# Performance work log

Hardware: AMD Instinct MI355X
Metric: run time of the kernel (lower is better)

The kernel has to match this reference:

```python
import jax, jax.numpy as jnp
import numpy as np

# Multi-level grid resolutions (module constants from init_kwargs)
RESO_3D = [16, 32, 64]
RESO_2D = [64, 128, 256]
EPS = 1e-9


def _corners(D):
    # binary corner offsets, shape (2**D, D)
    c = np.stack(np.meshgrid(*([np.arange(2)] * D), indexing='ij'), axis=-1).reshape(-1, D)
    return jnp.asarray(c, dtype=jnp.int32)


def _coords_weights(xyz, reso):
    # xyz in [0,1), shape (N, D). Returns flat voxel idx (N, 2**D) and trilinear weights (N, 2**D).
    D = xyz.shape[1]
    corners = _corners(D)                                   # (C, D)
    x = xyz * (reso - 1)
    x0 = jnp.floor(x)
    frac = x - x0                                           # (N, D)
    x0 = x0.astype(jnp.int32)
    cc = jnp.clip(x0[:, None, :] + corners[None], 0, reso - 1)   # (N, C, D)
    w = jnp.prod(jnp.where(corners[None] == 1, frac[:, None, :], 1.0 - frac[:, None, :]), axis=-1)  # (N, C)
    strides = (reso ** jnp.arange(D - 1, -1, -1)).astype(jnp.int32)  # row-major
    idx = jnp.sum(cc * strides, axis=-1)                    # (N, C)
    return idx, w


def _grid_create(xyz, feat, reso):
    # Scatter-splat: weighted-average point features into a dense level grid (reso**D, F).
    N, D = xyz.shape
    F = feat.shape[1]
    idx, w = _coords_weights(xyz, reso)                     # (N, C)
    flat_idx = idx.reshape(-1)
    wf = jnp.zeros((reso ** D, F), dtype=feat.dtype).at[flat_idx].add(
        (w[..., None] * feat[:, None, :]).reshape(-1, F))
    ws = jnp.zeros((reso ** D,), dtype=feat.dtype).at[flat_idx].add(w.reshape(-1))
    return wf / jnp.maximum(ws, EPS)[:, None]


def _grid_encode(xyz, grid, reso):
    # Gather + trilinear interpolation from a dense level grid. Returns (M, F).
    idx, w = _coords_weights(xyz, reso)                     # (M, C)
    vals = grid[idx]                                        # (M, C, F)
    return jnp.sum(w[..., None] * vals, axis=1)


def _spatial_ctx(xyz_c, xyz_i, feat):
    outs = []
    # 3D multi-level grid
    for R in RESO_3D:
        g = _grid_create(xyz_c, feat, R)
        outs.append(_grid_encode(xyz_i, g, R))
    # triplane 2D grids: xy, xz, yz
    for dims in ((0, 1), (0, 2), (1, 2)):
        xc = xyz_c[:, list(dims)]
        xi = xyz_i[:, list(dims)]
        for R in RESO_2D:
            g = _grid_create(xc, feat, R)
            outs.append(_grid_encode(xi, g, R))
    return jnp.concatenate(outs, axis=-1)  # (M, (L3 + 3*L2) * F)


def setup_inputs() -> dict:
    key = jax.random.key(0)
    k1, k2, k3 = jax.random.split(key, 3)
    N, M, F = 200000, 100000, 32
    xyz_for_creater = jax.random.uniform(k1, (N, 3), dtype=jnp.float32)
    xyz_for_interp = jax.random.uniform(k2, (M, 3), dtype=jnp.float32)
    feature = jax.random.normal(k3, (N, F), dtype=jnp.float32)
    return {"xyz_for_creater": xyz_for_creater,
            "xyz_for_interp": xyz_for_interp,
            "feature": feature}


def reference(xyz_for_creater, xyz_for_interp, feature):
    return _spatial_ctx(xyz_for_creater, xyz_for_interp, feature)
```

## Files before the change

### kernel.cpp

```cpp
#include <hip/hip_runtime.h>

#define NF 32
#define EPSF 1e-9f

#define KSORT 458752
#define KVIS 557056
#define KO16 0
#define KO32 4096
#define KO64 36864
#define KO64Q 299008
#define KO128Q 311296
#define KO256Q 360448

__device__ __forceinline__ int cell_coord(float xv, int R, float& fr) {
  float x = xv * (float)(R - 1);
  int i0 = (int)floorf(x);
  i0 = min(max(i0, 0), R - 2);
  fr = x - (float)i0;
  return i0;
}
__device__ __forceinline__ float bf2f(unsigned short u) {
  return __uint_as_float((unsigned)u << 16);
}
__device__ __forceinline__ unsigned short f2bf(float x) {
  unsigned b = __float_as_uint(x);
  return (unsigned short)((b + 0x7FFF + ((b >> 16) & 1)) >> 16);
}
__device__ __forceinline__ unsigned p1b2(unsigned x) {
  x &= 0x3FF;
  x = (x | (x << 16)) & 0x030000FF;
  x = (x | (x << 8)) & 0x0300F00F;
  x = (x | (x << 4)) & 0x030C30C3;
  x = (x | (x << 2)) & 0x09249249;
  return x;
}
__device__ __forceinline__ unsigned p1b1(unsigned x) {
  x &= 0xFFFF;
  x = (x | (x << 8)) & 0x00FF00FF;
  x = (x | (x << 4)) & 0x0F0F0F0F;
  x = (x | (x << 2)) & 0x33333333;
  x = (x | (x << 1)) & 0x55555555;
  return x;
}

__device__ __forceinline__ int xcd_swz(int bid, int n) {
  return (bid & 7) * (n >> 3) + (bid >> 3);
}

__device__ __forceinline__ void agg_hist(int key, int* cnt) {
  int lane = threadIdx.x & 63;
  unsigned long long amask = __ballot(1);
  int nact = __popcll(amask);
  int prev = __shfl_up(key, 1);
  bool leader = (lane == 0) || (prev != key);
  unsigned long long lmask = __ballot(leader);
  if (leader) {
    unsigned long long above = (lane < 63) ? (lmask >> (lane + 1)) : 0ULL;
    int next = above ? (lane + 1 + (__ffsll((unsigned long long)above) - 1)) : nact;
    atomicAdd(&cnt[key], next - lane);
  }
}

template <int NC>
__device__ __forceinline__ void agg_place_batch(const int (&key)[NC], int* cur,
                                                int (&pos)[NC]) {
  int lane = threadIdx.x & 63;
  unsigned long long amask = __ballot(1);
  int nact = __popcll(amask);
  int ret[NC];
  int lp[NC];
#pragma unroll
  for (int c = 0; c < NC; ++c) {
    int prev = __shfl_up(key[c], 1);
    bool leader = (lane == 0) || (prev != key[c]);
    unsigned long long lmask = __ballot(leader);
    unsigned long long below = lmask & ((2ULL << lane) - 1ULL);
    lp[c] = 63 - __clzll((long long)below);
    ret[c] = 0;
    if (leader) {
      unsigned long long above = (lane < 63) ? (lmask >> (lane + 1)) : 0ULL;
      int next = above ? (lane + 1 + (__ffsll((unsigned long long)above) - 1)) : nact;
      ret[c] = atomicAdd(&cur[key[c]], next - lane);
    }
  }
#pragma unroll
  for (int c = 0; c < NC; ++c) {
    pos[c] = __shfl(ret[c], lp[c]) + (lane - lp[c]);
  }
}

__global__ __launch_bounds__(256) void sort_hist_all(
    const float* __restrict__ xyz, int* __restrict__ cnt, int N) {
  int p = blockIdx.x * blockDim.x + threadIdx.x;
  if (p >= N) return;
  float fr;
  int c64[3], c256[3];
#pragma unroll
  for (int d = 0; d < 3; ++d) {
    c64[d] = cell_coord(xyz[p * 3 + d], 64, fr);
    c256[d] = cell_coord(xyz[p * 3 + d], 256, fr);
  }
  int k3 = (int)((p1b2((unsigned)c64[0]) << 2) | (p1b2((unsigned)c64[1]) << 1) |
                 p1b2((unsigned)c64[2]));
  atomicAdd(&cnt[k3], 1);
#pragma unroll
  for (int g = 0; g < 3; ++g) {
    int a = (g < 2) ? 0 : 1, b = (g == 0) ? 1 : 2;
    int key = 262144 + g * 65536 +
              (int)((p1b1((unsigned)c256[a]) << 1) | p1b1((unsigned)c256[b]));
    atomicAdd(&cnt[key], 1);
  }
}
__global__ __launch_bounds__(256) void sort_place_all(
    const float* __restrict__ xyz, int* __restrict__ cur, int* __restrict__ perm, int N) {
  int p = blockIdx.x * blockDim.x + threadIdx.x;
  if (p >= N) return;
  float fr;
  int c64[3], c256[3];
#pragma unroll
  for (int d = 0; d < 3; ++d) {
    c64[d] = cell_coord(xyz[p * 3 + d], 64, fr);
    c256[d] = cell_coord(xyz[p * 3 + d], 256, fr);
  }
  int k3 = (int)((p1b2((unsigned)c64[0]) << 2) | (p1b2((unsigned)c64[1]) << 1) |
                 p1b2((unsigned)c64[2]));
  perm[atomicAdd(&cur[k3], 1)] = p;
#pragma unroll
  for (int g = 0; g < 3; ++g) {
    int a = (g < 2) ? 0 : 1, b = (g == 0) ? 1 : 2;
    int key = 262144 + g * 65536 +
              (int)((p1b1((unsigned)c256[a]) << 1) | p1b1((unsigned)c256[b]));
    perm[atomicAdd(&cur[key], 1)] = p;
  }
}
__global__ __launch_bounds__(256) void permute_all(
    const float* __restrict__ xyz, const float* __restrict__ feat,
    const int* __restrict__ perm, float* __restrict__ xyz_s,
    unsigned short* __restrict__ feat_s, float* __restrict__ xy_g,
    unsigned short* __restrict__ feat_g, int N) {
  int t = blockIdx.x * blockDim.x + threadIdx.x;
  int s = t >> 5, f = t & 31;
  if (s >= 4 * N) return;
  int q = perm[s];
  float v = feat[(size_t)q * NF + f];
  if (s < N) {
    feat_s[(size_t)s * NF + f] = f2bf(v);
    if (f < 3) xyz_s[s * 3 + f] = xyz[q * 3 + f];
  } else {
    int sl = s - N;
    int g = sl / N;
    feat_g[(size_t)sl * NF + f] = f2bf(v);
    if (f < 2) {
      int a = (g < 2) ? 0 : 1, b = (g == 0) ? 1 : 2;
      xy_g[(size_t)sl * 2 + f] = xyz[q * 3 + (f == 0 ? a : b)];
    }
  }
}

__global__ __launch_bounds__(256) void scan_blocksum(
    const int* __restrict__ cnt, int* __restrict__ bsum, int K) {
  __shared__ int red[256];
  int base = blockIdx.x * 2048 + threadIdx.x * 8;
  int s = 0;
#pragma unroll
  for (int j = 0; j < 8; ++j) {
    int k = base + j;
    if (k < K) s += cnt[k];
  }
  red[threadIdx.x] = s;
  __syncthreads();
  for (int off = 128; off > 0; off >>= 1) {
    if (threadIdx.x < off) red[threadIdx.x] += red[threadIdx.x + off];
    __syncthreads();
  }
  if (threadIdx.x == 0) bsum[blockIdx.x] = red[0];
}
__global__ __launch_bounds__(256) void scan_write(
    const int* __restrict__ cnt, const int* __restrict__ bsum,
    int* __restrict__ cur, int K) {
  __shared__ int lds[256];
  __shared__ int boff;
  int b = blockIdx.x, t = threadIdx.x;
  if (t == 0) {
    int s = 0;
    for (int j = 0; j < b; ++j) s += bsum[j];
    boff = s;
  }
  int base = b * 2048 + t * 8;
  int v[8];
  int s = 0;
#pragma unroll
  for (int j = 0; j < 8; ++j) {
    int k = base + j;
    v[j] = (k < K) ? cnt[k] : 0;
    s += v[j];
  }
  lds[t] = s;
  __syncthreads();
  for (int off = 1; off < 256; off <<= 1) {
    int add = (t >= off) ? lds[t - off] : 0;
    __syncthreads();
    lds[t] += add;
    __syncthreads();
  }
  int run = boff + lds[t] - s;
#pragma unroll
  for (int j = 0; j < 8; ++j) {
    int k = base + j;
    if (k < K) {
      cur[k] = run;
      run += v[j];
    }
  }
}

template <int PHASE>
__global__ __launch_bounds__(256) void visit3_all(
    const float* __restrict__ xyz, int* __restrict__ cnt, int* __restrict__ cur,
    int2* __restrict__ visits, int N) {
  int r = blockIdx.y;
  int p = blockIdx.x * blockDim.x + threadIdx.x;
  if (p >= N) return;
  int R = 16 << r;
  int ko = (r == 0) ? KO16 : (r == 1 ? KO32 : KO64);
  unsigned a0[3], a1[3];
  float fr[3];
#pragma unroll
  for (int d = 0; d < 3; ++d) {
    int i0 = cell_coord(xyz[p * 3 + d], R, fr[d]);
    a0[d] = p1b2((unsigned)i0);
    a1[d] = p1b2((unsigned)(i0 + 1));
  }
  int keys[8];
  float ws[8];
#pragma unroll
  for (int cb = 0; cb < 8; ++cb) {
    float w = 1.f;
    unsigned key = 0;
#pragma unroll
    for (int d = 0; d < 3; ++d) {
      int o = (cb >> d) & 1;
      w *= o ? fr[d] : (1.f - fr[d]);
      key |= (o ? a1[d] : a0[d]) << (2 - d);
    }
    keys[cb] = ko + (int)key;
    ws[cb] = w;
  }
  if (PHASE == 0) {
#pragma unroll
    for (int cb = 0; cb < 8; ++cb) agg_hist(keys[cb], cnt);
  } else {
    int pos[8];
    agg_place_batch<8>(keys, cur, pos);
#pragma unroll
    for (int cb = 0; cb < 8; ++cb)
      visits[pos[cb]] = make_int2(p, __float_as_int(ws[cb]));
  }
}

template <int PHASE>
__global__ __launch_bounds__(256) void visit2_all(
    const float* __restrict__ xy_g, int* __restrict__ cnt, int* __restrict__ cur,
    int2* __restrict__ visits, int N) {
  int y = blockIdx.y;
  int g = y / 3, r = y % 3;
  int p = blockIdx.x * blockDim.x + threadIdx.x;
  if (p >= N) return;
  int sl = g * N + p;
  int R = 64 << r;
  int kb = (r == 0) ? KO64Q : (r == 1 ? KO128Q : KO256Q);
  int base = kb + g * R * R;
  float frx, fry;
  int ix = cell_coord(xy_g[(size_t)sl * 2 + 0], R, frx);
  int iy = cell_coord(xy_g[(size_t)sl * 2 + 1], R, fry);
  unsigned ax0 = p1b1((unsigned)ix), ax1 = p1b1((unsigned)(ix + 1));
  unsigned ay0 = p1b1((unsigned)iy), ay1 = p1b1((unsigned)(iy + 1));
  int keys[4];
  float ws[4];
#pragma unroll
  for (int cb = 0; cb < 4; ++cb) {
    int o0 = (cb >> 1) & 1, o1 = cb & 1;
    ws[cb] = (o0 ? frx : 1.f - frx) * (o1 ? fry : 1.f - fry);
    keys[cb] = base + (int)(((o0 ? ax1 : ax0) << 1) | (o1 ? ay1 : ay0));
  }
  if (PHASE == 0) {
#pragma unroll
    for (int cb = 0; cb < 4; ++cb) agg_hist(keys[cb], cnt);
  } else {
    int pos[4];
    agg_place_batch<4>(keys, cur, pos);
#pragma unroll
    for (int cb = 0; cb < 4; ++cb)
      visits[pos[cb]] = make_int2(sl, __float_as_int(ws[cb]));
  }
}

__global__ __launch_bounds__(256) void create_block(
    const unsigned short* __restrict__ feat, const int* __restrict__ cnt,
    const int* __restrict__ cur_end, const int2* __restrict__ visits,
    unsigned short* __restrict__ grid, int CBASE) {
  __shared__ int2 vlds[1024];
  __shared__ float2 lacc[256];
  __shared__ float lw[16];
  int cell = CBASE + xcd_swz(blockIdx.x, gridDim.x);
  int e = cur_end[cell];
  int n = cnt[cell];
  int beg = e - n;
  for (int i = threadIdx.x; i < n && i < 1024; i += 256) vlds[i] = visits[beg + i];
  __syncthreads();
  bool inl = (n <= 1024);
  int slot = threadIdx.x >> 4;
  int fp = threadIdx.x & 15;
  float2 acc = {0.f, 0.f};
  float wsum = 0.f;
  int i = slot;
  for (; i + 16 < n; i += 32) {
    int2 v0 = inl ? vlds[i] : visits[beg + i];
    int2 v1 = inl ? vlds[i + 16] : visits[beg + i + 16];
    unsigned u0 = *(const unsigned*)(feat + (size_t)v0.x * NF + 2 * fp);
    unsigned u1 = *(const unsigned*)(feat + (size_t)v1.x * NF + 2 * fp);
    float w0 = __int_as_float(v0.y), w1 = __int_as_float(v1.y);
    acc.x = fmaf(w0, bf2f((unsigned short)u0), acc.x);
    acc.y = fmaf(w0, bf2f((unsigned short)(u0 >> 16)), acc.y);
    acc.x = fmaf(w1, bf2f((unsigned short)u1), acc.x);
    acc.y = fmaf(w1, bf2f((unsigned short)(u1 >> 16)), acc.y);
    wsum += w0 + w1;
  }
  if (i < n) {
    int2 v = inl ? vlds[i] : visits[beg + i];
    unsigned u = *(const unsigned*)(feat + (size_t)v.x * NF + 2 * fp);
    float w = __int_as_float(v.y);
    acc.x = fmaf(w, bf2f((unsigned short)u), acc.x);
    acc.y = fmaf(w, bf2f((unsigned short)(u >> 16)), acc.y);
    wsum += w;
  }
  lacc[threadIdx.x] = acc;
  if (fp == 0) lw[slot] = wsum;
  __syncthreads();
  if (threadIdx.x < 16) {
    float2 a = {0.f, 0.f};
    float w = 0.f;
#pragma unroll
    for (int s = 0; s < 16; ++s) {
      float2 t = lacc[s * 16 + threadIdx.x];
      a.x += t.x;
      a.y += t.y;
      w += lw[s];
    }
    float inv = 1.f / fmaxf(w, EPSF);
    unsigned short lo = f2bf(a.x * inv), hi = f2bf(a.y * inv);
    *(unsigned*)(grid + (size_t)cell * NF + 2 * threadIdx.x) =
        (unsigned)lo | ((unsigned)hi << 16);
  }
}

__global__ __launch_bounds__(256) void create_wave4(
    const unsigned short* __restrict__ feat, const int* __restrict__ cnt,
    const int* __restrict__ cur_end, const int2* __restrict__ visits,
    unsigned short* __restrict__ grid, int CBASE, int K) {
  __shared__ int2 vlds[1024];
  int wave = threadIdx.x >> 6, lane = threadIdx.x & 63;
  int slot = lane >> 4;
  int fp = lane & 15;
  int c0 = CBASE + xcd_swz(blockIdx.x, gridDim.x) * 4;
  int lastc = min(c0 + 3, CBASE + K - 1);
  int vbase = cur_end[c0] - cnt[c0];
  int vlen = cur_end[lastc] - vbase;
  for (int i = threadIdx.x; i < vlen && i < 1024; i += 256) vlds[i] = visits[vbase + i];
  __syncthreads();
  int cell = c0 + wave;
  if (cell > lastc) return;
  int e = cur_end[cell];
  int n = cnt[cell];
  int beg = e - n;
  bool inl = (e - vbase) <= 1024;
  int b0 = beg - vbase;
  float2 acc = {0.f, 0.f};
  float wsum = 0.f;
  for (int i = slot; i < n; i += 4) {
    int2 v = inl ? vlds[b0 + i] : visits[beg + i];
    unsigned u = *(const unsigned*)(feat + (size_t)v.x * NF + 2 * fp);
    float w = __int_as_float(v.y);
    acc.x = fmaf(w, bf2f((unsigned short)u), acc.x);
    acc.y = fmaf(w, bf2f((unsigned short)(u >> 16)), acc.y);
    wsum += w;
  }
  acc.x += __shfl_xor(acc.x, 16);
  acc.y += __shfl_xor(acc.y, 16);
  wsum += __shfl_xor(wsum, 16);
  acc.x += __shfl_xor(acc.x, 32);
  acc.y += __shfl_xor(acc.y, 32);
  wsum += __shfl_xor(wsum, 32);
  if (slot == 0) {
    float inv = 1.f / fmaxf(wsum, EPSF);
    unsigned short lo = f2bf(acc.x * inv), hi = f2bf(acc.y * inv);
    *(unsigned*)(grid + (size_t)cell * NF + 2 * fp) =
        (unsigned)lo | ((unsigned)hi << 16);
  }
}

__global__ __launch_bounds__(256) void encode_all(
    const float* __restrict__ xyz, const unsigned short* __restrict__ grid,
    float* __restrict__ out, int M) {
  int t = blockIdx.x * blockDim.x + threadIdx.x;
  int m = t >> 5, f = t & 31;
  if (m >= M) return;
  float X[3];
#pragma unroll
  for (int d = 0; d < 3; ++d) X[d] = xyz[m * 3 + d];
  {
    const int RS[3] = {16, 32, 64};
    const int KO[3] = {KO16, KO32, KO64};
#pragma unroll
    for (int r = 0; r < 3; ++r) {
      unsigned a0[3], a1[3];
      float fr[3];
#pragma unroll
      for (int d = 0; d < 3; ++d) {
        int i0 = cell_coord(X[d], RS[r], fr[d]);
        a0[d] = p1b2((unsigned)i0);
        a1[d] = p1b2((unsigned)(i0 + 1));
      }
      float acc = 0.f;
#pragma unroll
      for (int cb = 0; cb < 8; ++cb) {
        float w = 1.f;
        unsigned key = 0;
#pragma unroll
        for (int d = 0; d < 3; ++d) {
          int o = (cb >> d) & 1;
          w *= o ? fr[d] : (1.f - fr[d]);
          key |= (o ? a1[d] : a0[d]) << (2 - d);
        }
        acc = fmaf(w, bf2f(grid[(size_t)(KO[r] + (int)key) * NF + f]), acc);
      }
      out[(size_t)m * 384 + r * 32 + f] = acc;
    }
  }
  {
    const int RS[3] = {64, 128, 256};
    const int KB[3] = {KO64Q, KO128Q, KO256Q};
    const int RSQ[3] = {4096, 16384, 65536};
#pragma unroll
    for (int r = 0; r < 3; ++r) {
      unsigned b0[3], b1[3];
      float fr[3];
#pragma unroll
      for (int d = 0; d < 3; ++d) {
        int i0 = cell_coord(X[d], RS[r], fr[d]);
        b0[d] = p1b1((unsigned)i0);
        b1[d] = p1b1((unsigned)(i0 + 1));
      }
#pragma unroll
      for (int g = 0; g < 3; ++g) {
        int a = (g < 2) ? 0 : 1, b = (g == 0) ? 1 : 2;
        int base = KB[r] + g * RSQ[r];
        float acc = 0.f;
#pragma unroll
        for (int cb = 0; cb < 4; ++cb) {
          int o0 = (cb >> 1) & 1, o1 = cb & 1;
          float w = (o0 ? fr[a] : 1.f - fr[a]) * (o1 ? fr[b] : 1.f - fr[b]);
          int k = base + (int)(((o0 ? b1[a] : b0[a]) << 1) | (o1 ? b1[b] : b0[b]));
          acc = fmaf(w, bf2f(grid[(size_t)k * NF + f]), acc);
        }
        out[(size_t)m * 384 + (3 + g * 3 + r) * 32 + f] = acc;
      }
    }
  }
}

extern "C" void kernel_launch(void* const* d_in, const int* in_sizes, int n_in,
                              void* d_out, int out_size, void* d_ws, size_t ws_size,
                              hipStream_t stream) {
  const float* xyz_c = (const float*)d_in[0];
  const float* xyz_i = (const float*)d_in[1];
  const float* feat = (const float*)d_in[2];
  float* out = (float*)d_out;
  int N = in_sizes[0] / 3;
  int M = in_sizes[1] / 3;

  char* wsb = (char*)d_ws;
  size_t off = 0;
  auto al = [&](size_t bytes) {
    size_t o = off;
    off = (off + bytes + 255) & ~(size_t)255;
    return wsb + o;
  };
  const int KALL = KSORT + KVIS;
  int* cnt_all = (int*)al((size_t)KALL * 4);
  int* cur_all = (int*)al((size_t)KALL * 4);
  int* bsum = (int*)al(4096);
  int* perm = (int*)al((size_t)4 * N * 4);
  float* xyz_s = (float*)al((size_t)N * 3 * 4);
  unsigned short* feat_s = (unsigned short*)al((size_t)N * NF * 2);
  float* xy_g = (float*)al((size_t)3 * N * 2 * 4);
  unsigned short* feat_g = (unsigned short*)al((size_t)3 * N * NF * 2);
  int2* visits = (int2*)al((size_t)60 * N * 8);
  unsigned short* grid = (unsigned short*)al((size_t)KVIS * NF * 2);

  int* cnt_v = cnt_all + KSORT;
  int* cur_v = cur_all + KSORT;

  int pb = (N + 255) / 256;
  int nbs = (KSORT + 2047) / 2048;
  int nbv = (KVIS + 2047) / 2048;

  hipMemsetAsync(cnt_all, 0, (size_t)KALL * 4, stream);

  sort_hist_all<<<pb, 256, 0, stream>>>(xyz_c, cnt_all, N);
  scan_blocksum<<<nbs, 256, 0, stream>>>(cnt_all, bsum, KSORT);
  scan_write<<<nbs, 256, 0, stream>>>(cnt_all, bsum, cur_all, KSORT);
  sort_place_all<<<pb, 256, 0, stream>>>(xyz_c, cur_all, perm, N);
  permute_all<<<(4 * N * 32 + 255) / 256, 256, 0, stream>>>(xyz_c, feat, perm, xyz_s,
                                                            feat_s, xy_g, feat_g, N);

  visit3_all<0><<<dim3(pb, 3), 256, 0, stream>>>(xyz_s, cnt_v, cur_v, visits, N);
  visit2_all<0><<<dim3(pb, 9), 256, 0, stream>>>(xy_g, cnt_v, cur_v, visits, N);
  scan_blocksum<<<nbv, 256, 0, stream>>>(cnt_v, bsum, KVIS);
  scan_write<<<nbv, 256, 0, stream>>>(cnt_v, bsum, cur_v, KVIS);
  visit3_all<1><<<dim3(pb, 3), 256, 0, stream>>>(xyz_s, cnt_v, cur_v, visits, N);
  visit2_all<1><<<dim3(pb, 9), 256, 0, stream>>>(xy_g, cnt_v, cur_v, visits, N);

  create_block<<<4096, 256, 0, stream>>>(feat_s, cnt_v, cur_v, visits, grid, KO16);
  create_block<<<32768, 256, 0, stream>>>(feat_s, cnt_v, cur_v, visits, grid, KO32);
  create_wave4<<<262144 / 4, 256, 0, stream>>>(feat_s, cnt_v, cur_v, visits, grid, KO64,
                                               262144);
  create_block<<<12288, 256, 0, stream>>>(feat_g, cnt_v, cur_v, visits, grid, KO64Q);
  create_block<<<49152, 256, 0, stream>>>(feat_g, cnt_v, cur_v, visits, grid, KO128Q);
  create_wave4<<<196608 / 4, 256, 0, stream>>>(feat_g, cnt_v, cur_v, visits, grid,
                                               KO256Q, 196608);

  encode_all<<<(M * 32 + 255) / 256, 256, 0, stream>>>(xyz_i, grid, out, M);
}
```

Before: 839.2 us.

## Derive finest-level visit lists from sort histogram via stencil instead of atomics

For the 64^3 and 256^2 levels, which match the sort keys, per-cell visit counts and per-corner-class offsets are now computed from the existing sort histogram by a neighbour stencil. Points then write their visits directly at offset plus rank within their sorted cell, so no atomics are needed. This removes the atomic histogram and atomic placement passes for the heaviest levels, at the cost of extra stencil kernels and offset buffers. Correctness relies on the points already being sorted by those cell keys and on the create_wave4 cur_start semantics lining up with the scan output.

```diff
diff --git a/kernel.cpp b/kernel.cpp
--- a/kernel.cpp
+++ b/kernel.cpp
@@ -40,6 +40,22 @@
   x = (x | (x << 4)) & 0x0F0F0F0F;
   x = (x | (x << 2)) & 0x33333333;
   x = (x | (x << 1)) & 0x55555555;
+  return x;
+}
+__device__ __forceinline__ unsigned c1b2(unsigned x) {
+  x &= 0x09249249u;
+  x = (x | (x >> 2)) & 0x030C30C3u;
+  x = (x | (x >> 4)) & 0x0300F00Fu;
+  x = (x | (x >> 8)) & 0x030000FFu;
+  x = (x | (x >> 16)) & 0x3FFu;
+  return x;
+}
+__device__ __forceinline__ unsigned c1b1(unsigned x) {
+  x &= 0x55555555u;
+  x = (x | (x >> 1)) & 0x33333333u;
+  x = (x | (x >> 2)) & 0x0F0F0F0Fu;
+  x = (x | (x >> 4)) & 0x00FF00FFu;
+  x = (x | (x >> 8)) & 0xFFFFu;
   return x;
 }
 
@@ -60,7 +76,6 @@
     atomicAdd(&cnt[key], next - lane);
   }
 }
-
 template <int NC>
 __device__ __forceinline__ void agg_place_batch(const int (&key)[NC], int* cur,
                                                 int (&pos)[NC]) {
@@ -84,9 +99,7 @@
     }
   }
 #pragma unroll
-  for (int c = 0; c < NC; ++c) {
-    pos[c] = __shfl(ret[c], lp[c]) + (lane - lp[c]);
-  }
+  for (int c = 0; c < NC; ++c) pos[c] = __shfl(ret[c], lp[c]) + (lane - lp[c]);
 }
 
 __global__ __launch_bounds__(256) void sort_hist_all(
@@ -215,14 +228,14 @@
 }
 
 template <int PHASE>
-__global__ __launch_bounds__(256) void visit3_all(
+__global__ __launch_bounds__(256) void visit3_coarse(
     const float* __restrict__ xyz, int* __restrict__ cnt, int* __restrict__ cur,
     int2* __restrict__ visits, int N) {
   int r = blockIdx.y;
   int p = blockIdx.x * blockDim.x + threadIdx.x;
   if (p >= N) return;
   int R = 16 << r;
-  int ko = (r == 0) ? KO16 : (r == 1 ? KO32 : KO64);
+  int ko = (r == 0) ? KO16 : KO32;
   unsigned a0[3], a1[3];
   float fr[3];
 #pragma unroll
@@ -259,16 +272,16 @@
 }
 
 template <int PHASE>
-__global__ __launch_bounds__(256) void visit2_all(
+__global__ __launch_bounds__(256) void visit2_coarse(
     const float* __restrict__ xy_g, int* __restrict__ cnt, int* __restrict__ cur,
     int2* __restrict__ visits, int N) {
   int y = blockIdx.y;
-  int g = y / 3, r = y % 3;
+  int g = y >> 1, r = y & 1;
   int p = blockIdx.x * blockDim.x + threadIdx.x;
   if (p >= N) return;
   int sl = g * N + p;
   int R = 64 << r;
-  int kb = (r == 0) ? KO64Q : (r == 1 ? KO128Q : KO256Q);
+  int kb = (r == 0) ? KO64Q : KO128Q;
   int base = kb + g * R * R;
   float frx, fry;
   int ix = cell_coord(xy_g[(size_t)sl * 2 + 0], R, frx);
@@ -292,6 +305,127 @@
 #pragma unroll
     for (int cb = 0; cb < 4; ++cb)
       visits[pos[cb]] = make_int2(sl, __float_as_int(ws[cb]));
+  }
+}
+
+__global__ __launch_bounds__(256) void stencilA64(const int* __restrict__ h64,
+                                                  int* __restrict__ cnt_v) {
+  int c = blockIdx.x * 256 + threadIdx.x;
+  int cx = (int)c1b2((unsigned)c >> 2), cy = (int)c1b2((unsigned)c >> 1),
+      cz = (int)c1b2((unsigned)c);
+  int s = 0;
+#pragma unroll
+  for (int cls = 0; cls < 8; ++cls) {
+    int hx = cx - (cls & 1), hy = cy - ((cls >> 1) & 1), hz = cz - ((cls >> 2) & 1);
+    if (hx < 0 || hy < 0 || hz < 0) continue;
+    int hk = (int)((p1b2((unsigned)hx) << 2) | (p1b2((unsigned)hy) << 1) |
+                   p1b2((unsigned)hz));
+    s += h64[hk];
+  }
+  cnt_v[KO64 + c] = s;
+}
+__global__ __launch_bounds__(256) void stencilB64(const int* __restrict__ h64,
+                                                  const int* __restrict__ cur_v,
+                                                  int* __restrict__ coff3) {
+  int c = blockIdx.x * 256 + threadIdx.x;
+  int cx = (int)c1b2((unsigned)c >> 2), cy = (int)c1b2((unsigned)c >> 1),
+      cz = (int)c1b2((unsigned)c);
+  int run = cur_v[KO64 + c];
+#pragma unroll
+  for (int cls = 0; cls < 8; ++cls) {
+    coff3[(size_t)c * 8 + cls] = run;
+    int hx = cx - (cls & 1), hy = cy - ((cls >> 1) & 1), hz = cz - ((cls >> 2) & 1);
+    if (hx < 0 || hy < 0 || hz < 0) continue;
+    int hk = (int)((p1b2((unsigned)hx) << 2) | (p1b2((unsigned)hy) << 1) |
+                   p1b2((unsigned)hz));
+    run += h64[hk];
+  }
+}
+__global__ __launch_bounds__(256) void stencilA256(const int* __restrict__ cnt_all,
+                                                   int* __restrict__ cnt_v) {
+  int t = blockIdx.x * 256 + threadIdx.x;
+  int g = t >> 16, m = t & 65535;
+  int cx = (int)c1b1((unsigned)m >> 1), cy = (int)c1b1((unsigned)m);
+  const int* h = cnt_all + 262144 + g * 65536;
+  int s = 0;
+#pragma unroll
+  for (int cls = 0; cls < 4; ++cls) {
+    int hx = cx - ((cls >> 1) & 1), hy = cy - (cls & 1);
+    if (hx < 0 || hy < 0) continue;
+    s += h[(int)((p1b1((unsigned)hx) << 1) | p1b1((unsigned)hy))];
+  }
+  cnt_v[KO256Q + t] = s;
+}
+__global__ __launch_bounds__(256) void stencilB256(const int* __restrict__ cnt_all,
+                                                   const int* __restrict__ cur_v,
+                                                   int* __restrict__ coff2) {
+  int t = blockIdx.x * 256 + threadIdx.x;
+  int g = t >> 16, m = t & 65535;
+  int cx = (int)c1b1((unsigned)m >> 1), cy = (int)c1b1((unsigned)m);
+  const int* h = cnt_all + 262144 + g * 65536;
+  int run = cur_v[KO256Q + t];
+#pragma unroll
+  for (int cls = 0; cls < 4; ++cls) {
+    coff2[(size_t)t * 4 + cls] = run;
+    int hx = cx - ((cls >> 1) & 1), hy = cy - (cls & 1);
+    if (hx < 0 || hy < 0) continue;
+    run += h[(int)((p1b1((unsigned)hx) << 1) | p1b1((unsigned)hy))];
+  }
+}
+
+__global__ __launch_bounds__(256) void emission64(
+    const float* __restrict__ xyz_s, const int* __restrict__ cnt_all,
+    const int* __restrict__ cur_ends, const int* __restrict__ coff3,
+    int2* __restrict__ visits, int N) {
+  int p = blockIdx.x * blockDim.x + threadIdx.x;
+  if (p >= N) return;
+  unsigned a0[3], a1[3];
+  float fr[3];
+#pragma unroll
+  for (int d = 0; d < 3; ++d) {
+    int i0 = cell_coord(xyz_s[p * 3 + d], 64, fr[d]);
+    a0[d] = p1b2((unsigned)i0);
+    a1[d] = p1b2((unsigned)(i0 + 1));
+  }
+  int hk = (int)((a0[0] << 2) | (a0[1] << 1) | a0[2]);
+  int rank = p - (cur_ends[hk] - cnt_all[hk]);
+#pragma unroll
+  for (int cb = 0; cb < 8; ++cb) {
+    float w = 1.f;
+    unsigned key = 0;
+#pragma unroll
+    for (int d = 0; d < 3; ++d) {
+      int o = (cb >> d) & 1;
+      w *= o ? fr[d] : (1.f - fr[d]);
+      key |= (o ? a1[d] : a0[d]) << (2 - d);
+    }
+    int pos = coff3[(size_t)key * 8 + cb] + rank;
+    visits[pos] = make_int2(p, __float_as_int(w));
+  }
+}
+__global__ __launch_bounds__(256) void emission256(
+    const float* __restrict__ xy_g, const int* __restrict__ cnt_all,
+    const int* __restrict__ cur_ends, const int* __restrict__ coff2,
+    int2* __restrict__ visits, int N) {
+  int g = blockIdx.y;
+  int p = blockIdx.x * blockDim.x + threadIdx.x;
+  if (p >= N) return;
+  int sl = g * N + p;
+  float frx, fry;
+  int ix = cell_coord(xy_g[(size_t)sl * 2 + 0], 256, frx);
+  int iy = cell_coord(xy_g[(size_t)sl * 2 + 1], 256, fry);
+  unsigned ax0 = p1b1((unsigned)ix), ax1 = p1b1((unsigned)(ix + 1));
+  unsigned ay0 = p1b1((unsigned)iy), ay1 = p1b1((unsigned)(iy + 1));
+  int m = (int)((ax0 << 1) | ay0);
+  int sk = 262144 + g * 65536 + m;
+  int rank = sl - (cur_ends[sk] - cnt_all[sk] - N);
+#pragma unroll
+  for (int cb = 0; cb < 4; ++cb) {
+    int o0 = (cb >> 1) & 1, o1 = cb & 1;
+    float w = (o0 ? frx : 1.f - frx) * (o1 ? fry : 1.f - fry);
+    int key = (int)(((o0 ? ax1 : ax0) << 1) | (o1 ? ay1 : ay0));
+    int pos = coff2[(size_t)(g * 65536 + key) * 4 + cb] + rank;
+    visits[pos] = make_int2(sl, __float_as_int(w));
   }
 }
 
@@ -356,7 +490,7 @@
 
 __global__ __launch_bounds__(256) void create_wave4(
     const unsigned short* __restrict__ feat, const int* __restrict__ cnt,
-    const int* __restrict__ cur_end, const int2* __restrict__ visits,
+    const int* __restrict__ cur_start, const int2* __restrict__ visits,
     unsigned short* __restrict__ grid, int CBASE, int K) {
   __shared__ int2 vlds[1024];
   int wave = threadIdx.x >> 6, lane = threadIdx.x & 63;
@@ -364,16 +498,15 @@
   int fp = lane & 15;
   int c0 = CBASE + xcd_swz(blockIdx.x, gridDim.x) * 4;
   int lastc = min(c0 + 3, CBASE + K - 1);
-  int vbase = cur_end[c0] - cnt[c0];
-  int vlen = cur_end[lastc] - vbase;
+  int vbase = cur_start[c0];
+  int vlen = cur_start[lastc] + cnt[lastc] - vbase;
   for (int i = threadIdx.x; i < vlen && i < 1024; i += 256) vlds[i] = visits[vbase + i];
   __syncthreads();
   int cell = c0 + wave;
   if (cell > lastc) return;
-  int e = cur_end[cell];
+  int beg = cur_start[cell];
   int n = cnt[cell];
-  int beg = e - n;
-  bool inl = (e - vbase) <= 1024;
+  bool inl = (beg + n - vbase) <= 1024;
   int b0 = beg - vbase;
   float2 acc = {0.f, 0.f};
   float wsum = 0.f;
@@ -497,6 +630,8 @@
   unsigned short* feat_g = (unsigned short*)al((size_t)3 * N * NF * 2);
   int2* visits = (int2*)al((size_t)60 * N * 8);
   unsigned short* grid = (unsigned short*)al((size_t)KVIS * NF * 2);
+  int* coff3 = (int*)al((size_t)262144 * 8 * 4);
+  int* coff2 = (int*)al((size_t)196608 * 4 * 4);
 
   int* cnt_v = cnt_all + KSORT;
   int* cur_v = cur_all + KSORT;
@@ -514,12 +649,19 @@
   permute_all<<<(4 * N * 32 + 255) / 256, 256, 0, stream>>>(xyz_c, feat, perm, xyz_s,
                                                             feat_s, xy_g, feat_g, N);
 
-  visit3_all<0><<<dim3(pb, 3), 256, 0, stream>>>(xyz_s, cnt_v, cur_v, visits, N);
-  visit2_all<0><<<dim3(pb, 9), 256, 0, stream>>>(xy_g, cnt_v, cur_v, visits, N);
+  visit3_coarse<0><<<dim3(pb, 2), 256, 0, stream>>>(xyz_s, cnt_v, cur_v, visits, N);
+  visit2_coarse<0><<<dim3(pb, 6), 256, 0, stream>>>(xy_g, cnt_v, cur_v, visits, N);
+  stencilA64<<<262144 / 256, 256, 0, stream>>>(cnt_all, cnt_v);
+  stencilA256<<<196608 / 256, 256, 0, stream>>>(cnt_all, cnt_v);
   scan_blocksum<<<nbv, 256, 0, stream>>>(cnt_v, bsum, KVIS);
   scan_write<<<nbv, 256, 0, stream>>>(cnt_v, bsum, cur_v, KVIS);
-  visit3_all<1><<<dim3(pb, 3), 256, 0, stream>>>(xyz_s, cnt_v, cur_v, visits, N);
-  visit2_all<1><<<dim3(pb, 9), 256, 0, stream>>>(xy_g, cnt_v, cur_v, visits, N);
+  stencilB64<<<262144 / 256, 256, 0, stream>>>(cnt_all, cur_v, coff3);
+  stencilB256<<<196608 / 256, 256, 0, stream>>>(cnt_all, cur_v, coff2);
+
+  visit3_coarse<1><<<dim3(pb, 2), 256, 0, stream>>>(xyz_s, cnt_v, cur_v, visits, N);
+  visit2_coarse<1><<<dim3(pb, 6), 256, 0, stream>>>(xy_g, cnt_v, cur_v, visits, N);
+  emission64<<<pb, 256, 0, stream>>>(xyz_s, cnt_all, cur_all, coff3, visits, N);
+  emission256<<<dim3(pb, 3), 256, 0, stream>>>(xy_g, cnt_all, cur_all, coff2, visits, N);
 
   create_block<<<4096, 256, 0, stream>>>(feat_s, cnt_v, cur_v, visits, grid, KO16);
   create_block<<<32768, 256, 0, stream>>>(feat_s, cnt_v, cur_v, visits, grid, KO32);
```

Result: no change. 842.1 us (+0.3%).
